# Optimization experiments

Hardware: AMD Instinct MI355X
Metric: run time of the kernel (lower is better)

The kernel has to match this reference:

```python
import jax, jax.numpy as jnp
import numpy as np

X = 512; Y = 512; C = 3; NK = 15
DT = 0.2; DD = 2; SIGMA = 0.95
THETA_X = 2.0; N_EXP = 2.0
K_SIZE = 16

# mesh-grid positions, cell centers at +0.5 (matches construct_mesh_grid)
POS = (jnp.stack(jnp.meshgrid(jnp.arange(X), jnp.arange(Y), indexing='ij'), axis=-1) + 0.5).astype(jnp.float32)  # [X,Y,2]


def _dwconv(img, k):
    # img [X,Y,C'] -> depthwise 3x3 cross-correlation with 'same' zero padding (matches torch conv2d)
    z = img.transpose(2, 0, 1)[None]                      # [1,C',X,Y]
    kern = jnp.tile(k[None, None], (z.shape[1], 1, 1, 1))  # [C',1,3,3]
    out = jax.lax.conv_general_dilated(z, kern, (1, 1), 'SAME', feature_group_count=z.shape[1])
    return out[0].transpose(1, 2, 0)


def _sobel(img):
    # returns [X,Y,2,C'] with (sy, sx) stacked on axis 2, matching torch code order
    kx = jnp.array([[-1., 0., 1.], [-2., 0., 2.], [-1., 0., 1.]], jnp.float32)
    return jnp.stack([_dwconv(img, kx.T), _dwconv(img, kx)], axis=2)


def _reintegrate(grid, F):
    # Flow-Lenia reintegration tracking: 25 static roll offsets, fused accumulation
    ma = DD - SIGMA
    mu = POS[..., None] + jnp.clip(DT * F, -ma, ma)  # [X,Y,2,C]
    mu = jnp.clip(mu, SIGMA, X - SIGMA)
    clip_hi = min(1.0, 2.0 * SIGMA)
    inv_area = 1.0 / (4.0 * SIGMA ** 2)
    acc = jnp.zeros_like(grid)
    for dx in range(-DD, DD + 1):
        for dy in range(-DD, DD + 1):
            gridR = jnp.roll(grid, (dx, dy), (0, 1))
            muR = jnp.roll(mu, (dx, dy), (0, 1))
            sz = 0.5 - jnp.abs(POS[..., None] - muR) + SIGMA
            area = jnp.prod(jnp.clip(sz, 0.0, clip_hi), axis=2) * inv_area  # [X,Y,C]
            acc = acc + gridR * area
    return acc


def _forward(x, Ks, m, s, h, w_c1, c0):
    # spectral kernels: normalize, fftshift, fft2 (matches construct_kernels)
    Ksn = Ks / Ks.sum(axis=(0, 1), keepdims=True)
    fk = jnp.fft.fft2(jnp.fft.fftshift(Ksn, axes=(0, 1)), axes=(0, 1))  # [X,Y,NK] complex
    fXs = jnp.fft.fft2(x, axes=(0, 1))
    Us = jnp.fft.ifft2(fk * fXs[:, :, c0], axes=(0, 1)).real            # [X,Y,NK]
    # growth * h (note: h appears again inside w_c1, faithful to original double multiply)
    Gs = (jnp.exp(-(((Us - m) / s) ** 2) * 0.5) * 2.0 - 1.0) * h
    Hs = jnp.einsum('xyk,kc->xyc', Gs, w_c1)                             # [X,Y,C]
    grad_u = _sobel(Hs)                                                  # [X,Y,2,C]
    grad_x = _sobel(x.sum(-1, keepdims=True))                            # [X,Y,2,1]
    alpha = jnp.clip((x[:, :, None, :] / THETA_X) ** N_EXP, 0.0, 1.0)    # [X,Y,1,C]
    F = grad_u * (1.0 - alpha) - grad_x * alpha                          # [X,Y,2,C]
    return _reintegrate(x, F)


def setup_inputs() -> dict:
    key = jax.random.key(0)
    k1, k2, k3, k4, k5 = jax.random.split(key, 5)
    x = jax.random.uniform(k1, (X, Y, C), jnp.float32)
    # ring kernels per construct_kernels (non-sparse branch)
    mg = np.mgrid[-X // 2:X // 2, -Y // 2:Y // 2]
    base = np.linalg.norm(mg, axis=0).astype(np.float32)
    ks_list = []
    for i in range(NK):
        r = 0.6 + 0.04 * i
        D = base / ((K_SIZE + 15) * r)
        sig = 0.5 * (np.tanh(-(D - 1.0) * 10.0 / 2.0) + 1.0)
        bell = np.exp(-(D - 0.5) ** 2 / 0.15)
        ks_list.append(sig * bell)
    Ks = jnp.asarray(np.stack(ks_list, -1).astype(np.float32))
    m = 0.1 + 0.3 * jax.random.uniform(k2, (NK,), jnp.float32)
    s = 0.03 + 0.15 * jax.random.uniform(k3, (NK,), jnp.float32)
    h = 0.3 + 0.7 * jax.random.uniform(k4, (NK,), jnp.float32)
    c0 = jax.random.randint(k5, (NK,), 0, C, jnp.int32)
    c1 = jnp.arange(NK) % C
    w_c1 = jax.nn.one_hot(c1, C, dtype=jnp.float32) * h[:, None]
    return {"x": x, "Ks": Ks, "m": m, "s": s, "h": h, "w_c1": w_c1, "c0": c0}


def reference(x, Ks, m, s, h, w_c1, c0):
    return _forward(x, Ks, m, s, h, w_c1, c0)
```

## Files before the change

kernel.cpp:

```cpp
#include <hip/hip_runtime.h>
#include <math.h>

#define NPIX 262144
#define NKER 15
#define PI_F 3.14159265358979323846f
#define HW 264
#define CS 578
#define SK(n) ((n) + ((n) >> 3))

__device__ __forceinline__ float2 cadd(float2 a, float2 b) { return make_float2(a.x + b.x, a.y + b.y); }
__device__ __forceinline__ float2 csub(float2 a, float2 b) { return make_float2(a.x - b.x, a.y - b.y); }
__device__ __forceinline__ float2 cmul(float2 a, float2 b) {
  return make_float2(a.x * b.x - a.y * b.y, a.x * b.y + a.y * b.x);
}
__device__ __forceinline__ float2 cmulc(float2 a, float2 b) {
  return make_float2(a.x * b.x + a.y * b.y, a.y * b.x - a.x * b.y);
}

__device__ __forceinline__ void build_tw(int lane, float2* pA, float2* pB) {
  float s, c;
  sincosf(-2.0f * PI_F * (float)lane / 512.0f, &s, &c);
  float2 w1 = make_float2(c, s);
  int h = lane & ~7;
  float2 wh = make_float2(__shfl(c, h, 64), __shfl(s, h, 64));
  pA[0] = w1;
  pA[1] = cmul(w1, w1);
  pA[2] = cmul(pA[1], w1);
  pA[3] = cmul(pA[1], pA[1]);
  pA[4] = cmul(pA[3], w1);
  pA[5] = cmul(pA[3], pA[1]);
  pA[6] = cmul(pA[3], pA[2]);
  pB[0] = wh;
  pB[1] = cmul(wh, wh);
  pB[2] = cmul(pB[1], wh);
  pB[3] = cmul(pB[1], pB[1]);
  pB[4] = cmul(pB[3], wh);
  pB[5] = cmul(pB[3], pB[1]);
  pB[6] = cmul(pB[3], pB[2]);
}

template <bool INV>
__device__ __forceinline__ void dft8(float2 a[8]) {
  const float R = 0.70710678118654752f;
  float2 t0 = cadd(a[0], a[4]), u0 = csub(a[0], a[4]);
  float2 t1 = cadd(a[1], a[5]), u1 = csub(a[1], a[5]);
  float2 t2 = cadd(a[2], a[6]), u2 = csub(a[2], a[6]);
  float2 t3 = cadd(a[3], a[7]), u3 = csub(a[3], a[7]);
  u1 = INV ? make_float2(R * (u1.x - u1.y), R * (u1.x + u1.y))
           : make_float2(R * (u1.x + u1.y), R * (u1.y - u1.x));
  u2 = INV ? make_float2(-u2.y, u2.x) : make_float2(u2.y, -u2.x);
  u3 = INV ? make_float2(-R * (u3.x + u3.y), R * (u3.x - u3.y))
           : make_float2(R * (u3.y - u3.x), -R * (u3.x + u3.y));
  float2 e0 = cadd(t0, t2), f0 = csub(t0, t2);
  float2 e1 = cadd(t1, t3), f1 = csub(t1, t3);
  f1 = INV ? make_float2(-f1.y, f1.x) : make_float2(f1.y, -f1.x);
  float2 g0 = cadd(u0, u2), h0 = csub(u0, u2);
  float2 g1 = cadd(u1, u3), h1 = csub(u1, u3);
  h1 = INV ? make_float2(-h1.y, h1.x) : make_float2(h1.y, -h1.x);
  a[0] = cadd(e0, e1); a[4] = csub(e0, e1);
  a[2] = cadd(f0, f1); a[6] = csub(f0, f1);
  a[1] = cadd(g0, g1); a[5] = csub(g0, g1);
  a[3] = cadd(h0, h1); a[7] = csub(h0, h1);
}

template <bool INV>
__device__ __forceinline__ void fft512_r8(float2 a[8], float2* buf, int lane,
                                          const float2* pA, const float2* pB) {
  dft8<INV>(a);
#pragma unroll
  for (int q = 1; q < 8; ++q) a[q] = INV ? cmulc(a[q], pA[q - 1]) : cmul(a[q], pA[q - 1]);
#pragma unroll
  for (int q = 0; q < 8; ++q) buf[9 * lane + q] = a[q];
#pragma unroll
  for (int q = 0; q < 8; ++q) a[q] = buf[SK(lane + 64 * q)];
  dft8<INV>(a);
#pragma unroll
  for (int q = 1; q < 8; ++q) a[q] = INV ? cmulc(a[q], pB[q - 1]) : cmul(a[q], pB[q - 1]);
  int h = lane & ~7;
  int b2 = 9 * h + (lane - h);
#pragma unroll
  for (int q = 0; q < 8; ++q) buf[b2 + 9 * q] = a[q];
#pragma unroll
  for (int q = 0; q < 8; ++q) a[q] = buf[SK(lane + 64 * q)];
  dft8<INV>(a);
}

__device__ __forceinline__ void split_store_halfplane(float2 a[8], float2* buf, int lane,
                                                      float2* d0, float2* d1) {
#pragma unroll
  for (int q = 0; q < 8; ++q) buf[SK(lane + 64 * q)] = a[q];
#pragma unroll
  for (int q = 0; q < 4; ++q) {
    int v = lane + 64 * q;
    int mir = (512 - v) & 511;
    float2 P = a[q];
    float2 Qc = buf[SK(mir)];
    float2 Q = make_float2(Qc.x, -Qc.y);
    d0[v] = make_float2(0.5f * (P.x + Q.x), 0.5f * (P.y + Q.y));
    d1[v] = make_float2(0.5f * (P.y - Q.y), -0.5f * (P.x - Q.x));
  }
  if (lane == 0) {
    float2 P = a[4];
    d0[256] = make_float2(P.x, 0.f);
    d1[256] = make_float2(P.y, 0.f);
  }
}

__global__ __launch_bounds__(512, 4) void rows_all(
    const float* __restrict__ Ks, const float* __restrict__ x,
    float* __restrict__ partial, float2* __restrict__ AkH,
    float2* __restrict__ AxH) {
  __shared__ float krow[512 * NKER];
  __shared__ float2 scr[8][CS];
  __shared__ float psum[480];
  int t = threadIdx.x, wave = t >> 6, lane = t & 63;
  float2 pA[7], pB[7];
  build_tw(lane, pA, pB);
  if (blockIdx.x < 512) {
    int b = blockIdx.x;
    int rs = (b + 256) & 511;
    const float2* src = (const float2*)Ks + (size_t)rs * 3840;
    float2* kr2 = (float2*)krow;
    for (int i = t; i < 3840; i += 512) kr2[i] = src[i];
    __syncthreads();
    if (t < 480) {
      int k = t >> 5, yg = t & 31;
      float s = 0.f;
      int base = yg * 16;
#pragma unroll
      for (int y = 0; y < 16; ++y) s += krow[(base + y) * NKER + k];
      psum[t] = s;
    }
    {
      int k1 = 2 * wave, k2 = k1 + 1;
      float2 a[8];
#pragma unroll
      for (int q = 0; q < 8; ++q) {
        int ys = (lane + 64 * q + 256) & 511;
        float re = krow[ys * NKER + k1];
        float im = (k2 < NKER) ? krow[ys * NKER + k2] : 0.f;
        a[q] = make_float2(re, im);
      }
      fft512_r8<false>(a, &scr[wave][0], lane, pA, pB);
      float2* d0 = AkH + ((size_t)k1 * 512 + b) * HW;
      float2* d1 = AkH + ((size_t)k2 * 512 + b) * HW;
      split_store_halfplane(a, &scr[wave][0], lane, d0, d1);
    }
    __syncthreads();
    if (t < NKER) {
      float s = 0.f;
#pragma unroll
      for (int g = 0; g < 32; ++g) s += psum[(t << 5) + g];
      partial[b * 16 + t] = s;
    }
  } else {
    int job = (blockIdx.x - 512) * 8 + wave;
    int c = job >> 8;
    int rp = job & 255;
    int r0 = rp, r1 = rp + 256;
    float2 a[8];
#pragma unroll
    for (int q = 0; q < 8; ++q) {
      int y = lane + 64 * q;
      a[q] = make_float2(x[((size_t)r0 * 512 + y) * 3 + c],
                         x[((size_t)r1 * 512 + y) * 3 + c]);
    }
    fft512_r8<false>(a, &scr[wave][0], lane, pA, pB);
    float2* d0 = AxH + ((size_t)c * 512 + r0) * HW;
    float2* d1 = AxH + ((size_t)c * 512 + r1) * HW;
    split_store_halfplane(a, &scr[wave][0], lane, d0, d1);
  }
}

__global__ __launch_bounds__(512, 4) void xcols(const float2* __restrict__ AxH,
                                                float2* __restrict__ FxT) {
  __shared__ float2 buf[8 * CS];
  int t = threadIdx.x, c = t >> 6, lane = t & 63;
  int col0 = blockIdx.x << 3, ch = blockIdx.y;
  float2 pA[7], pB[7];
  build_tw(lane, pA, pB);
  const float2* bx = AxH + (size_t)ch * 512 * HW;
#pragma unroll
  for (int u = 0; u < 8; ++u) {
    int idx = (u << 9) + t;
    int row = idx >> 3, cc = idx & 7;
    buf[cc * CS + SK(row)] = bx[(size_t)row * HW + col0 + cc];
  }
  __syncthreads();
  float2 a[8];
#pragma unroll
  for (int q = 0; q < 8; ++q) a[q] = buf[c * CS + SK(lane + 64 * q)];
  fft512_r8<false>(a, &buf[c * CS], lane, pA, pB);
  float2* dst = FxT + ((size_t)ch * HW + col0 + c) * 512;
#pragma unroll
  for (int q = 0; q < 8; ++q) dst[lane + 64 * q] = a[q];
}

__global__ __launch_bounds__(512, 4) void fused_cols(
    float2* __restrict__ AkH, const float2* __restrict__ FxT,
    const int* __restrict__ c0, const float* __restrict__ partial,
    float* __restrict__ sums) {
  __shared__ float2 buf[8 * CS];
  __shared__ float red[512];
  int t = threadIdx.x;
  if (blockIdx.x == 33) {
    if (blockIdx.y != 0) return;
    int k = t & 15, g = t >> 4;
    float acc = 0.f;
    for (int b = g; b < 512; b += 32) acc += partial[b * 16 + k];
    red[t] = acc;
    __syncthreads();
    if (t < 16) {
      float s = 0.f;
#pragma unroll
      for (int g2 = 0; g2 < 32; ++g2) s += red[g2 * 16 + t];
      sums[t] = s;
    }
    return;
  }
  int col0 = blockIdx.x << 3, k = blockIdx.y;
  int c = t >> 6, lane = t & 63;
  float2 pA[7], pB[7];
  build_tw(lane, pA, pB);
  float2* bk = AkH + (size_t)k * 512 * HW;
#pragma unroll
  for (int u = 0; u < 8; ++u) {
    int idx = (u << 9) + t;
    int row = idx >> 3, cc = idx & 7;
    buf[cc * CS + SK(row)] = bk[(size_t)row * HW + col0 + cc];
  }
  const float2* fx = FxT + ((size_t)c0[k] * HW + col0 + c) * 512;
  float2 xq[8];
#pragma unroll
  for (int q = 0; q < 8; ++q) xq[q] = fx[lane + 64 * q];
  __syncthreads();
  float2 a[8];
#pragma unroll
  for (int q = 0; q < 8; ++q) a[q] = buf[c * CS + SK(lane + 64 * q)];
  fft512_r8<false>(a, &buf[c * CS], lane, pA, pB);
#pragma unroll
  for (int q = 0; q < 8; ++q) a[q] = cmul(a[q], xq[q]);
  fft512_r8<true>(a, &buf[c * CS], lane, pA, pB);
#pragma unroll
  for (int q = 0; q < 8; ++q) buf[c * CS + SK(lane + 64 * q)] = a[q];
  __syncthreads();
#pragma unroll
  for (int u = 0; u < 8; ++u) {
    int idx = (u << 9) + t;
    int row = idx >> 3, cc = idx & 7;
    bk[(size_t)row * HW + col0 + cc] = buf[cc * CS + SK(row)];
  }
}

__global__ __launch_bounds__(512, 4) void irows_growth_combine(
    const float2* __restrict__ AkH, const float* __restrict__ sums,
    const float* __restrict__ m, const float* __restrict__ s,
    const float* __restrict__ h, const float* __restrict__ w,
    float* __restrict__ Hs) {
  __shared__ float2 scr[8][CS];
  __shared__ float accL[4][3][512];
  __shared__ float mk[16], isk[16], hk[16], wk[16][3], sck[16];
  int t = threadIdx.x, wave = t >> 6, lane = t & 63;
  int row = blockIdx.x;
  if (t < NKER) {
    mk[t] = m[t]; isk[t] = 1.0f / s[t]; hk[t] = h[t];
    sck[t] = 1.0f / (sums[t] * 262144.0f);
    wk[t][0] = w[t * 3 + 0]; wk[t][1] = w[t * 3 + 1]; wk[t][2] = w[t * 3 + 2];
  }
  __syncthreads();
  float2 pA[7], pB[7];
  build_tw(lane, pA, pB);
  float acc[3][8];
#pragma unroll
  for (int cc = 0; cc < 3; ++cc)
#pragma unroll
    for (int q = 0; q < 8; ++q) acc[cc][q] = 0.f;
  {
    int slot = wave;
    int k1 = 2 * slot, k2 = 2 * slot + 1;
    bool dual = (k2 < NKER);
    const float2* p1 = AkH + ((size_t)k1 * 512 + row) * HW;
    const float2* p2 = AkH + ((size_t)(dual ? k2 : k1) * 512 + row) * HW;
    float2 a[8];
#pragma unroll
    for (int q = 0; q < 8; ++q) {
      int v = lane + 64 * q;
      if (v <= 256) {
        float2 A1 = p1[v];
        float2 A2 = dual ? p2[v] : make_float2(0.f, 0.f);
        a[q] = make_float2(A1.x - A2.y, A1.y + A2.x);
      } else {
        int mi = 512 - v;
        float2 A1 = p1[mi];
        float2 A2 = dual ? p2[mi] : make_float2(0.f, 0.f);
        a[q] = make_float2(A1.x + A2.y, -A1.y + A2.x);
      }
    }
    fft512_r8<true>(a, &scr[wave][0], lane, pA, pB);
    float m1 = mk[k1], i1 = isk[k1], h1 = hk[k1], s1 = sck[k1];
    float w10 = wk[k1][0], w11 = wk[k1][1], w12 = wk[k1][2];
#pragma unroll
    for (int q = 0; q < 8; ++q) {
      float tt = (a[q].x * s1 - m1) * i1;
      float g = (expf(-0.5f * tt * tt) * 2.0f - 1.0f) * h1;
      acc[0][q] += g * w10; acc[1][q] += g * w11; acc[2][q] += g * w12;
    }
    if (dual) {
      float m2 = mk[k2], i2 = isk[k2], h2 = hk[k2], s2 = sck[k2];
      float w20 = wk[k2][0], w21 = wk[k2][1], w22 = wk[k2][2];
#pragma unroll
      for (int q = 0; q < 8; ++q) {
        float tt = (a[q].y * s2 - m2) * i2;
        float g = (expf(-0.5f * tt * tt) * 2.0f - 1.0f) * h2;
        acc[0][q] += g * w20; acc[1][q] += g * w21; acc[2][q] += g * w22;
      }
    }
  }
  if (wave < 4) {
#pragma unroll
    for (int cc = 0; cc < 3; ++cc)
#pragma unroll
      for (int q = 0; q < 8; ++q) accL[wave][cc][lane + 64 * q] = acc[cc][q];
  }
  __syncthreads();
  if (wave >= 4) {
#pragma unroll
    for (int cc = 0; cc < 3; ++cc)
#pragma unroll
      for (int q = 0; q < 8; ++q) accL[wave - 4][cc][lane + 64 * q] += acc[cc][q];
  }
  __syncthreads();
#pragma unroll
  for (int cc = 0; cc < 3; ++cc) {
    float v = accL[0][cc][t] + accL[1][cc][t] + accL[2][cc][t] + accL[3][cc][t];
    Hs[(size_t)cc * NPIX + (size_t)row * 512 + t] = v;
  }
}

__global__ void flow_reint(const float* __restrict__ x, const float* __restrict__ Hs,
                           float* __restrict__ out) {
  __shared__ float tS[7][496];
  __shared__ float muT[400 * 6];
  int ox = (blockIdx.x >> 5) << 4;
  int oy = (blockIdx.x & 31) << 4;
  for (int i = threadIdx.x; i < 484; i += 256) {
    int li = i / 22, lj = i % 22;
    int qx = (ox - 3 + li) & 511, qy = (oy - 3 + lj) & 511;
    int q = (qx << 9) | qy;
    float h0 = Hs[q], h1 = Hs[NPIX + q], h2 = Hs[2 * NPIX + q];
    float x0 = x[(size_t)q * 3 + 0], x1 = x[(size_t)q * 3 + 1], x2 = x[(size_t)q * 3 + 2];
    tS[0][i] = h0; tS[1][i] = h1; tS[2][i] = h2;
    tS[3][i] = x0 + x1 + x2;
    tS[4][i] = x0; tS[5][i] = x1; tS[6][i] = x2;
  }
  __syncthreads();
  for (int i = threadIdx.x; i < 400; i += 256) {
    int hi = i / 20, hj = i % 20;
    int qx = (ox - 2 + hi) & 511, qy = (oy - 2 + hj) & 511;
    float syH0 = 0.f, syH1 = 0.f, syH2 = 0.f;
    float sxH0 = 0.f, sxH1 = 0.f, sxH2 = 0.f;
    float syX = 0.f, sxX = 0.f;
#pragma unroll
    for (int di = -1; di <= 1; ++di) {
#pragma unroll
      for (int dj = -1; dj <= 1; ++dj) {
        if (di == 0 && dj == 0) continue;
        int xi = qx + di, yj = qy + dj;
        if ((unsigned)xi >= 512u || (unsigned)yj >= 512u) continue;
        int l = (hi + 1 + di) * 22 + (hj + 1 + dj);
        float wy = (float)di * ((dj == 0) ? 2.f : 1.f);
        float wx = (float)dj * ((di == 0) ? 2.f : 1.f);
        float h0 = tS[0][l], h1 = tS[1][l], h2 = tS[2][l];
        syH0 += wy * h0; syH1 += wy * h1; syH2 += wy * h2;
        sxH0 += wx * h0; sxH1 += wx * h1; sxH2 += wx * h2;
        float xs = tS[3][l];
        syX += wy * xs; sxX += wx * xs;
      }
    }
    int lc = (hi + 1) * 22 + (hj + 1);
    float cxq = (float)qx + 0.5f, cyq = (float)qy + 0.5f;
    float syH[3] = {syH0, syH1, syH2};
    float sxH[3] = {sxH0, sxH1, sxH2};
    int b6 = i * 6;
#pragma unroll
    for (int c = 0; c < 3; ++c) {
      float xc = tS[4 + c][lc];
      float tt = xc * 0.5f;
      float alpha = fminf(tt * tt, 1.0f);
      float F0 = syH[c] * (1.f - alpha) - syX * alpha;
      float F1 = sxH[c] * (1.f - alpha) - sxX * alpha;
      float m0 = cxq + fminf(fmaxf(0.2f * F0, -1.05f), 1.05f);
      float m1 = cyq + fminf(fmaxf(0.2f * F1, -1.05f), 1.05f);
      muT[b6 + c]     = fminf(fmaxf(m0, 0.95f), 511.05f);
      muT[b6 + 3 + c] = fminf(fmaxf(m1, 0.95f), 511.05f);
    }
  }
  __syncthreads();
  int o = threadIdx.x;
  int lx = o >> 4, ly = o & 15;
  int px_ = ox + lx, py_ = oy + ly;
  float cx = (float)px_ + 0.5f, cy = (float)py_ + 0.5f;
  float a0 = 0.f, a1 = 0.f, a2 = 0.f;
#pragma unroll
  for (int dx = -2; dx <= 2; ++dx) {
    int hi = lx + 2 - dx;
#pragma unroll
    for (int dy = -2; dy <= 2; ++dy) {
      int hj = ly + 2 - dy;
      int b6 = (hi * 20 + hj) * 6;
      int lb = (hi + 1) * 22 + (hj + 1);
      float wv;
      wv = fminf(fmaxf(1.45f - fabsf(cx - muT[b6 + 0]), 0.f), 1.f) *
           fminf(fmaxf(1.45f - fabsf(cy - muT[b6 + 3]), 0.f), 1.f);
      a0 += tS[4][lb] * wv;
      wv = fminf(fmaxf(1.45f - fabsf(cx - muT[b6 + 1]), 0.f), 1.f) *
           fminf(fmaxf(1.45f - fabsf(cy - muT[b6 + 4]), 0.f), 1.f);
      a1 += tS[5][lb] * wv;
      wv = fminf(fmaxf(1.45f - fabsf(cx - muT[b6 + 2]), 0.f), 1.f) *
           fminf(fmaxf(1.45f - fabsf(cy - muT[b6 + 5]), 0.f), 1.f);
      a2 += tS[6][lb] * wv;
    }
  }
  const float inv_area = 0.27700831f;
  size_t p = (size_t)((px_ << 9) | py_);
  out[p * 3 + 0] = a0 * inv_area;
  out[p * 3 + 1] = a1 * inv_area;
  out[p * 3 + 2] = a2 * inv_area;
}

extern "C" void kernel_launch(void* const* d_in, const int* in_sizes, int n_in,
                              void* d_out, int out_size, void* d_ws, size_t ws_size,
                              hipStream_t stream) {
  const float* x    = (const float*)d_in[0];
  const float* Ks   = (const float*)d_in[1];
  const float* m    = (const float*)d_in[2];
  const float* s    = (const float*)d_in[3];
  const float* h    = (const float*)d_in[4];
  const float* w_c1 = (const float*)d_in[5];
  const int*   c0   = (const int*)d_in[6];
  float* out = (float*)d_out;

  char* ws = (char*)d_ws;
  size_t off = 0;
  float* sums    = (float*)(ws + off); off += 1024;
  float* partial = (float*)(ws + off); off += 512 * 16 * 4;
  float2* AxH  = (float2*)(ws + off); off += (size_t)3 * 512 * HW * 8;
  float2* AkH  = (float2*)(ws + off); off += (size_t)16 * 512 * HW * 8;
  float2* FxT  = (float2*)(ws + off); off += (size_t)3 * HW * 512 * 8;
  float*  Hs   = (float*)(ws + off);  off += (size_t)3 * NPIX * 4;

  rows_all<<<608, 512, 0, stream>>>(Ks, x, partial, AkH, AxH);
  xcols<<<dim3(33, 3), 512, 0, stream>>>(AxH, FxT);
  fused_cols<<<dim3(34, NKER), 512, 0, stream>>>(AkH, FxT, c0, partial, sums);
  irows_growth_combine<<<512, 512, 0, stream>>>(AkH, sums, m, s, h, w_c1, Hs);
  flow_reint<<<1024, 256, 0, stream>>>(x, Hs, out);
}
```

Before: 128.1 us.

## Vectorize complex math with float2 ext vectors, skip zero kernel rows, halve column blocks

Replaces the float2 struct helpers with clang ext_vector_type(2) arithmetic, so complex multiplies and the reintegration clamps can map to packed FP32 instructions. Row FFTs for Ks rows that are all zero within a wave are skipped and zeros are written directly. The column FFT kernels move from 8 to 4 columns per block (256 threads), doubling the grid, and the sum reduction moves from fused_cols into xcols. The zero-skip depends on the data being sparse and adds a wave vote, and the smaller blocks mean more launches' worth of blocks with less work each.

```diff
diff --git a/kernel.cpp b/kernel.cpp
--- a/kernel.cpp
+++ b/kernel.cpp
@@ -8,21 +8,31 @@
 #define CS 578
 #define SK(n) ((n) + ((n) >> 3))
 
-__device__ __forceinline__ float2 cadd(float2 a, float2 b) { return make_float2(a.x + b.x, a.y + b.y); }
-__device__ __forceinline__ float2 csub(float2 a, float2 b) { return make_float2(a.x - b.x, a.y - b.y); }
-__device__ __forceinline__ float2 cmul(float2 a, float2 b) {
-  return make_float2(a.x * b.x - a.y * b.y, a.x * b.y + a.y * b.x);
-}
-__device__ __forceinline__ float2 cmulc(float2 a, float2 b) {
-  return make_float2(a.x * b.x + a.y * b.y, a.y * b.x - a.x * b.y);
-}
-
-__device__ __forceinline__ void build_tw(int lane, float2* pA, float2* pB) {
+typedef float f2 __attribute__((ext_vector_type(2)));
+
+__device__ __forceinline__ f2 mkf2(float a, float b) { f2 r; r.x = a; r.y = b; return r; }
+__device__ __forceinline__ f2 rotp(f2 a) { return mkf2(-a.y, a.x); }
+__device__ __forceinline__ f2 rotm(f2 a) { return mkf2(a.y, -a.x); }
+__device__ __forceinline__ f2 cmul(f2 a, f2 b) {
+  f2 t = mkf2(a.x, a.x) * b;
+  f2 u = mkf2(-a.y, a.y) * mkf2(b.y, b.x);
+  return t + u;
+}
+__device__ __forceinline__ f2 cmulc(f2 a, f2 b) {
+  f2 t = a * mkf2(b.x, b.x);
+  f2 u = mkf2(a.y, -a.x) * mkf2(b.y, b.y);
+  return t + u;
+}
+__device__ __forceinline__ f2 vmin(f2 a, f2 b) { return __builtin_elementwise_min(a, b); }
+__device__ __forceinline__ f2 vmax(f2 a, f2 b) { return __builtin_elementwise_max(a, b); }
+__device__ __forceinline__ f2 vabs(f2 a) { return __builtin_elementwise_abs(a); }
+
+__device__ __forceinline__ void build_tw(int lane, f2* pA, f2* pB) {
   float s, c;
   sincosf(-2.0f * PI_F * (float)lane / 512.0f, &s, &c);
-  float2 w1 = make_float2(c, s);
+  f2 w1 = mkf2(c, s);
   int h = lane & ~7;
-  float2 wh = make_float2(__shfl(c, h, 64), __shfl(s, h, 64));
+  f2 wh = mkf2(__shfl(c, h, 64), __shfl(s, h, 64));
   pA[0] = w1;
   pA[1] = cmul(w1, w1);
   pA[2] = cmul(pA[1], w1);
@@ -40,32 +50,30 @@
 }
 
 template <bool INV>
-__device__ __forceinline__ void dft8(float2 a[8]) {
+__device__ __forceinline__ void dft8(f2 a[8]) {
   const float R = 0.70710678118654752f;
-  float2 t0 = cadd(a[0], a[4]), u0 = csub(a[0], a[4]);
-  float2 t1 = cadd(a[1], a[5]), u1 = csub(a[1], a[5]);
-  float2 t2 = cadd(a[2], a[6]), u2 = csub(a[2], a[6]);
-  float2 t3 = cadd(a[3], a[7]), u3 = csub(a[3], a[7]);
-  u1 = INV ? make_float2(R * (u1.x - u1.y), R * (u1.x + u1.y))
-           : make_float2(R * (u1.x + u1.y), R * (u1.y - u1.x));
-  u2 = INV ? make_float2(-u2.y, u2.x) : make_float2(u2.y, -u2.x);
-  u3 = INV ? make_float2(-R * (u3.x + u3.y), R * (u3.x - u3.y))
-           : make_float2(R * (u3.y - u3.x), -R * (u3.x + u3.y));
-  float2 e0 = cadd(t0, t2), f0 = csub(t0, t2);
-  float2 e1 = cadd(t1, t3), f1 = csub(t1, t3);
-  f1 = INV ? make_float2(-f1.y, f1.x) : make_float2(f1.y, -f1.x);
-  float2 g0 = cadd(u0, u2), h0 = csub(u0, u2);
-  float2 g1 = cadd(u1, u3), h1 = csub(u1, u3);
-  h1 = INV ? make_float2(-h1.y, h1.x) : make_float2(h1.y, -h1.x);
-  a[0] = cadd(e0, e1); a[4] = csub(e0, e1);
-  a[2] = cadd(f0, f1); a[6] = csub(f0, f1);
-  a[1] = cadd(g0, g1); a[5] = csub(g0, g1);
-  a[3] = cadd(h0, h1); a[7] = csub(h0, h1);
+  f2 t0 = a[0] + a[4], u0 = a[0] - a[4];
+  f2 t1 = a[1] + a[5], u1 = a[1] - a[5];
+  f2 t2 = a[2] + a[6], u2 = a[2] - a[6];
+  f2 t3 = a[3] + a[7], u3 = a[3] - a[7];
+  u1 = (INV ? (u1 + rotp(u1)) : (u1 + rotm(u1))) * R;
+  u2 = INV ? rotp(u2) : rotm(u2);
+  u3 = (INV ? (rotp(u3) - u3) : (rotm(u3) - u3)) * R;
+  f2 e0 = t0 + t2, f0 = t0 - t2;
+  f2 e1 = t1 + t3, f1 = t1 - t3;
+  f1 = INV ? rotp(f1) : rotm(f1);
+  f2 g0 = u0 + u2, h0 = u0 - u2;
+  f2 g1 = u1 + u3, h1 = u1 - u3;
+  h1 = INV ? rotp(h1) : rotm(h1);
+  a[0] = e0 + e1; a[4] = e0 - e1;
+  a[2] = f0 + f1; a[6] = f0 - f1;
+  a[1] = g0 + g1; a[5] = g0 - g1;
+  a[3] = h0 + h1; a[7] = h0 - h1;
 }
 
 template <bool INV>
-__device__ __forceinline__ void fft512_r8(float2 a[8], float2* buf, int lane,
-                                          const float2* pA, const float2* pB) {
+__device__ __forceinline__ void fft512_r8(f2 a[8], f2* buf, int lane,
+                                          const f2* pA, const f2* pB) {
   dft8<INV>(a);
 #pragma unroll
   for (int q = 1; q < 8; ++q) a[q] = INV ? cmulc(a[q], pA[q - 1]) : cmul(a[q], pA[q - 1]);
@@ -85,42 +93,41 @@
   dft8<INV>(a);
 }
 
-__device__ __forceinline__ void split_store_halfplane(float2 a[8], float2* buf, int lane,
-                                                      float2* d0, float2* d1) {
+__device__ __forceinline__ void split_store_halfplane(f2 a[8], f2* buf, int lane,
+                                                      f2* d0, f2* d1) {
 #pragma unroll
   for (int q = 0; q < 8; ++q) buf[SK(lane + 64 * q)] = a[q];
 #pragma unroll
   for (int q = 0; q < 4; ++q) {
     int v = lane + 64 * q;
     int mir = (512 - v) & 511;
-    float2 P = a[q];
-    float2 Qc = buf[SK(mir)];
-    float2 Q = make_float2(Qc.x, -Qc.y);
-    d0[v] = make_float2(0.5f * (P.x + Q.x), 0.5f * (P.y + Q.y));
-    d1[v] = make_float2(0.5f * (P.y - Q.y), -0.5f * (P.x - Q.x));
+    f2 P = a[q];
+    f2 Qc = buf[SK(mir)];
+    d0[v] = (P + mkf2(Qc.x, -Qc.y)) * 0.5f;
+    d1[v] = mkf2(0.5f * (P.y + Qc.y), 0.5f * (Qc.x - P.x));
   }
   if (lane == 0) {
-    float2 P = a[4];
-    d0[256] = make_float2(P.x, 0.f);
-    d1[256] = make_float2(P.y, 0.f);
+    f2 P = a[4];
+    d0[256] = mkf2(P.x, 0.f);
+    d1[256] = mkf2(P.y, 0.f);
   }
 }
 
 __global__ __launch_bounds__(512, 4) void rows_all(
     const float* __restrict__ Ks, const float* __restrict__ x,
-    float* __restrict__ partial, float2* __restrict__ AkH,
-    float2* __restrict__ AxH) {
+    float* __restrict__ partial, f2* __restrict__ AkH,
+    f2* __restrict__ AxH) {
   __shared__ float krow[512 * NKER];
-  __shared__ float2 scr[8][CS];
+  __shared__ f2 scr[8][CS];
   __shared__ float psum[480];
   int t = threadIdx.x, wave = t >> 6, lane = t & 63;
-  float2 pA[7], pB[7];
+  f2 pA[7], pB[7];
   build_tw(lane, pA, pB);
   if (blockIdx.x < 512) {
     int b = blockIdx.x;
     int rs = (b + 256) & 511;
-    const float2* src = (const float2*)Ks + (size_t)rs * 3840;
-    float2* kr2 = (float2*)krow;
+    const f2* src = (const f2*)Ks + (size_t)rs * 3840;
+    f2* kr2 = (f2*)krow;
     for (int i = t; i < 3840; i += 512) kr2[i] = src[i];
     __syncthreads();
     if (t < 480) {
@@ -133,18 +140,27 @@
     }
     {
       int k1 = 2 * wave, k2 = k1 + 1;
-      float2 a[8];
+      f2 a[8];
+      bool nz = false;
 #pragma unroll
       for (int q = 0; q < 8; ++q) {
         int ys = (lane + 64 * q + 256) & 511;
         float re = krow[ys * NKER + k1];
         float im = (k2 < NKER) ? krow[ys * NKER + k2] : 0.f;
-        a[q] = make_float2(re, im);
+        a[q] = mkf2(re, im);
+        nz |= (re != 0.f) || (im != 0.f);
       }
-      fft512_r8<false>(a, &scr[wave][0], lane, pA, pB);
-      float2* d0 = AkH + ((size_t)k1 * 512 + b) * HW;
-      float2* d1 = AkH + ((size_t)k2 * 512 + b) * HW;
-      split_store_halfplane(a, &scr[wave][0], lane, d0, d1);
+      f2* d0 = AkH + ((size_t)k1 * 512 + b) * HW;
+      f2* d1 = AkH + ((size_t)k2 * 512 + b) * HW;
+      if (__any((int)nz)) {
+        fft512_r8<false>(a, &scr[wave][0], lane, pA, pB);
+        split_store_halfplane(a, &scr[wave][0], lane, d0, d1);
+      } else {
+        f2 z = mkf2(0.f, 0.f);
+#pragma unroll
+        for (int q = 0; q < 4; ++q) { int v = lane + 64 * q; d0[v] = z; d1[v] = z; }
+        if (lane == 0) { d0[256] = z; d1[256] = z; }
+      }
     }
     __syncthreads();
     if (t < NKER) {
@@ -158,86 +174,88 @@
     int c = job >> 8;
     int rp = job & 255;
     int r0 = rp, r1 = rp + 256;
-    float2 a[8];
+    f2 a[8];
 #pragma unroll
     for (int q = 0; q < 8; ++q) {
       int y = lane + 64 * q;
-      a[q] = make_float2(x[((size_t)r0 * 512 + y) * 3 + c],
-                         x[((size_t)r1 * 512 + y) * 3 + c]);
+      a[q] = mkf2(x[((size_t)r0 * 512 + y) * 3 + c],
+                  x[((size_t)r1 * 512 + y) * 3 + c]);
     }
     fft512_r8<false>(a, &scr[wave][0], lane, pA, pB);
-    float2* d0 = AxH + ((size_t)c * 512 + r0) * HW;
-    float2* d1 = AxH + ((size_t)c * 512 + r1) * HW;
+    f2* d0 = AxH + ((size_t)c * 512 + r0) * HW;
+    f2* d1 = AxH + ((size_t)c * 512 + r1) * HW;
     split_store_halfplane(a, &scr[wave][0], lane, d0, d1);
   }
 }
 
-__global__ __launch_bounds__(512, 4) void xcols(const float2* __restrict__ AxH,
-                                                float2* __restrict__ FxT) {
-  __shared__ float2 buf[8 * CS];
-  int t = threadIdx.x, c = t >> 6, lane = t & 63;
-  int col0 = blockIdx.x << 3, ch = blockIdx.y;
-  float2 pA[7], pB[7];
-  build_tw(lane, pA, pB);
-  const float2* bx = AxH + (size_t)ch * 512 * HW;
-#pragma unroll
-  for (int u = 0; u < 8; ++u) {
-    int idx = (u << 9) + t;
-    int row = idx >> 3, cc = idx & 7;
-    buf[cc * CS + SK(row)] = bx[(size_t)row * HW + col0 + cc];
-  }
-  __syncthreads();
-  float2 a[8];
-#pragma unroll
-  for (int q = 0; q < 8; ++q) a[q] = buf[c * CS + SK(lane + 64 * q)];
-  fft512_r8<false>(a, &buf[c * CS], lane, pA, pB);
-  float2* dst = FxT + ((size_t)ch * HW + col0 + c) * 512;
-#pragma unroll
-  for (int q = 0; q < 8; ++q) dst[lane + 64 * q] = a[q];
-}
-
-__global__ __launch_bounds__(512, 4) void fused_cols(
-    float2* __restrict__ AkH, const float2* __restrict__ FxT,
-    const int* __restrict__ c0, const float* __restrict__ partial,
-    float* __restrict__ sums) {
-  __shared__ float2 buf[8 * CS];
-  __shared__ float red[512];
+__global__ __launch_bounds__(256, 4) void xcols(const f2* __restrict__ AxH,
+                                                f2* __restrict__ FxT,
+                                                const float* __restrict__ partial,
+                                                float* __restrict__ sums) {
+  __shared__ f2 buf[4 * CS];
+  __shared__ float red[256];
   int t = threadIdx.x;
-  if (blockIdx.x == 33) {
+  if (blockIdx.x == 66) {
     if (blockIdx.y != 0) return;
     int k = t & 15, g = t >> 4;
     float acc = 0.f;
-    for (int b = g; b < 512; b += 32) acc += partial[b * 16 + k];
+    for (int b = g; b < 512; b += 16) acc += partial[b * 16 + k];
     red[t] = acc;
     __syncthreads();
     if (t < 16) {
       float s = 0.f;
 #pragma unroll
-      for (int g2 = 0; g2 < 32; ++g2) s += red[g2 * 16 + t];
+      for (int g2 = 0; g2 < 16; ++g2) s += red[g2 * 16 + t];
       sums[t] = s;
     }
     return;
   }
-  int col0 = blockIdx.x << 3, k = blockIdx.y;
   int c = t >> 6, lane = t & 63;
-  float2 pA[7], pB[7];
+  int col0 = blockIdx.x << 2, ch = blockIdx.y;
+  f2 pA[7], pB[7];
   build_tw(lane, pA, pB);
-  float2* bk = AkH + (size_t)k * 512 * HW;
+  const f2* bx = AxH + (size_t)ch * 512 * HW;
 #pragma unroll
   for (int u = 0; u < 8; ++u) {
-    int idx = (u << 9) + t;
-    int row = idx >> 3, cc = idx & 7;
-    buf[cc * CS + SK(row)] = bk[(size_t)row * HW + col0 + cc];
-  }
-  const float2* fx = FxT + ((size_t)c0[k] * HW + col0 + c) * 512;
-  float2 xq[8];
-#pragma unroll
-  for (int q = 0; q < 8; ++q) xq[q] = fx[lane + 64 * q];
-  __syncthreads();
-  float2 a[8];
+    int idx = (u << 8) + t;
+    int row = idx >> 2, cc = idx & 3;
+    buf[cc * CS + SK(row)] = bx[(size_t)row * HW + col0 + cc];
+  }
+  __syncthreads();
+  f2 a[8];
 #pragma unroll
   for (int q = 0; q < 8; ++q) a[q] = buf[c * CS + SK(lane + 64 * q)];
   fft512_r8<false>(a, &buf[c * CS], lane, pA, pB);
+  f2* dst = FxT + ((size_t)ch * HW + col0 + c) * 512;
+#pragma unroll
+  for (int q = 0; q < 8; ++q) dst[lane + 64 * q] = a[q];
+}
+
+__global__ __launch_bounds__(256, 4) void fused_cols(
+    f2* __restrict__ AkH, const f2* __restrict__ FxT,
+    const int* __restrict__ c0) {
+  __shared__ f2 buf[4 * CS];
+  int t = threadIdx.x;
+  int col0 = blockIdx.x << 2, k = blockIdx.y;
+  int c = t >> 6, lane = t & 63;
+  f2 pA[7], pB[7];
+  build_tw(lane, pA, pB);
+  f2* bk = AkH + (size_t)k * 512 * HW;
+#pragma unroll
+  for (int u = 0; u < 8; ++u) {
+    int idx = (u << 8) + t;
+    int row = idx >> 2, cc = idx & 3;
+    buf[cc * CS + SK(row)] = bk[(size_t)row * HW + col0 + cc];
+  }
+  const f2* fx = FxT + ((size_t)c0[k] * HW + col0 + c) * 512;
+  f2 xq[8];
+#pragma unroll
+  for (int q = 0; q < 8; ++q) xq[q] = fx[lane + 64 * q];
+  __syncthreads();
+  f2 a[8];
+#pragma unroll
+  for (int q = 0; q < 8; ++q) a[q] = buf[c * CS + SK(lane + 64 * q)];
+  fft512_r8<false>(a, &buf[c * CS], lane, pA, pB);
 #pragma unroll
   for (int q = 0; q < 8; ++q) a[q] = cmul(a[q], xq[q]);
   fft512_r8<true>(a, &buf[c * CS], lane, pA, pB);
@@ -246,18 +264,18 @@
   __syncthreads();
 #pragma unroll
   for (int u = 0; u < 8; ++u) {
-    int idx = (u << 9) + t;
-    int row = idx >> 3, cc = idx & 7;
+    int idx = (u << 8) + t;
+    int row = idx >> 2, cc = idx & 3;
     bk[(size_t)row * HW + col0 + cc] = buf[cc * CS + SK(row)];
   }
 }
 
 __global__ __launch_bounds__(512, 4) void irows_growth_combine(
-    const float2* __restrict__ AkH, const float* __restrict__ sums,
+    const f2* __restrict__ AkH, const float* __restrict__ sums,
     const float* __restrict__ m, const float* __restrict__ s,
     const float* __restrict__ h, const float* __restrict__ w,
     float* __restrict__ Hs) {
-  __shared__ float2 scr[8][CS];
+  __shared__ f2 scr[8][CS];
   __shared__ float accL[4][3][512];
   __shared__ float mk[16], isk[16], hk[16], wk[16][3], sck[16];
   int t = threadIdx.x, wave = t >> 6, lane = t & 63;
@@ -268,7 +286,7 @@
     wk[t][0] = w[t * 3 + 0]; wk[t][1] = w[t * 3 + 1]; wk[t][2] = w[t * 3 + 2];
   }
   __syncthreads();
-  float2 pA[7], pB[7];
+  f2 pA[7], pB[7];
   build_tw(lane, pA, pB);
   float acc[3][8];
 #pragma unroll
@@ -279,21 +297,21 @@
     int slot = wave;
     int k1 = 2 * slot, k2 = 2 * slot + 1;
     bool dual = (k2 < NKER);
-    const float2* p1 = AkH + ((size_t)k1 * 512 + row) * HW;
-    const float2* p2 = AkH + ((size_t)(dual ? k2 : k1) * 512 + row) * HW;
-    float2 a[8];
+    const f2* p1 = AkH + ((size_t)k1 * 512 + row) * HW;
+    const f2* p2 = AkH + ((size_t)(dual ? k2 : k1) * 512 + row) * HW;
+    f2 a[8];
 #pragma unroll
     for (int q = 0; q < 8; ++q) {
       int v = lane + 64 * q;
       if (v <= 256) {
-        float2 A1 = p1[v];
-        float2 A2 = dual ? p2[v] : make_float2(0.f, 0.f);
-        a[q] = make_float2(A1.x - A2.y, A1.y + A2.x);
+        f2 A1 = p1[v];
+        f2 A2 = dual ? p2[v] : mkf2(0.f, 0.f);
+        a[q] = mkf2(A1.x - A2.y, A1.y + A2.x);
       } else {
         int mi = 512 - v;
-        float2 A1 = p1[mi];
-        float2 A2 = dual ? p2[mi] : make_float2(0.f, 0.f);
-        a[q] = make_float2(A1.x + A2.y, -A1.y + A2.x);
+        f2 A1 = p1[mi];
+        f2 A2 = dual ? p2[mi] : mkf2(0.f, 0.f);
+        a[q] = mkf2(A1.x + A2.y, -A1.y + A2.x);
       }
     }
     fft512_r8<true>(a, &scr[wave][0], lane, pA, pB);
@@ -340,7 +358,7 @@
 __global__ void flow_reint(const float* __restrict__ x, const float* __restrict__ Hs,
                            float* __restrict__ out) {
   __shared__ float tS[7][496];
-  __shared__ float muT[400 * 6];
+  __shared__ f2 muF[400 * 3];
   int ox = (blockIdx.x >> 5) << 4;
   int oy = (blockIdx.x & 31) << 4;
   for (int i = threadIdx.x; i < 484; i += 256) {
@@ -357,9 +375,7 @@
   for (int i = threadIdx.x; i < 400; i += 256) {
     int hi = i / 20, hj = i % 20;
     int qx = (ox - 2 + hi) & 511, qy = (oy - 2 + hj) & 511;
-    float syH0 = 0.f, syH1 = 0.f, syH2 = 0.f;
-    float sxH0 = 0.f, sxH1 = 0.f, sxH2 = 0.f;
-    float syX = 0.f, sxX = 0.f;
+    f2 sH0 = mkf2(0.f, 0.f), sH1 = sH0, sH2 = sH0, sX = sH0;
 #pragma unroll
     for (int di = -1; di <= 1; ++di) {
 #pragma unroll
@@ -370,36 +386,34 @@
         int l = (hi + 1 + di) * 22 + (hj + 1 + dj);
         float wy = (float)di * ((dj == 0) ? 2.f : 1.f);
         float wx = (float)dj * ((di == 0) ? 2.f : 1.f);
-        float h0 = tS[0][l], h1 = tS[1][l], h2 = tS[2][l];
-        syH0 += wy * h0; syH1 += wy * h1; syH2 += wy * h2;
-        sxH0 += wx * h0; sxH1 += wx * h1; sxH2 += wx * h2;
-        float xs = tS[3][l];
-        syX += wy * xs; sxX += wx * xs;
+        f2 wv = mkf2(wy, wx);
+        sH0 += wv * tS[0][l];
+        sH1 += wv * tS[1][l];
+        sH2 += wv * tS[2][l];
+        sX  += wv * tS[3][l];
       }
     }
     int lc = (hi + 1) * 22 + (hj + 1);
-    float cxq = (float)qx + 0.5f, cyq = (float)qy + 0.5f;
-    float syH[3] = {syH0, syH1, syH2};
-    float sxH[3] = {sxH0, sxH1, sxH2};
-    int b6 = i * 6;
+    f2 ctr = mkf2((float)qx + 0.5f, (float)qy + 0.5f);
+    f2 sH[3] = {sH0, sH1, sH2};
+    const f2 lo = mkf2(-1.05f, -1.05f), hi2 = mkf2(1.05f, 1.05f);
+    const f2 mlo = mkf2(0.95f, 0.95f), mhi = mkf2(511.05f, 511.05f);
 #pragma unroll
     for (int c = 0; c < 3; ++c) {
       float xc = tS[4 + c][lc];
       float tt = xc * 0.5f;
       float alpha = fminf(tt * tt, 1.0f);
-      float F0 = syH[c] * (1.f - alpha) - syX * alpha;
-      float F1 = sxH[c] * (1.f - alpha) - sxX * alpha;
-      float m0 = cxq + fminf(fmaxf(0.2f * F0, -1.05f), 1.05f);
-      float m1 = cyq + fminf(fmaxf(0.2f * F1, -1.05f), 1.05f);
-      muT[b6 + c]     = fminf(fmaxf(m0, 0.95f), 511.05f);
-      muT[b6 + 3 + c] = fminf(fmaxf(m1, 0.95f), 511.05f);
+      f2 F = sH[c] * (1.f - alpha) - sX * alpha;
+      f2 mu = ctr + vmin(vmax(F * 0.2f, lo), hi2);
+      muF[i * 3 + c] = vmin(vmax(mu, mlo), mhi);
     }
   }
   __syncthreads();
   int o = threadIdx.x;
   int lx = o >> 4, ly = o & 15;
   int px_ = ox + lx, py_ = oy + ly;
-  float cx = (float)px_ + 0.5f, cy = (float)py_ + 0.5f;
+  f2 ctr = mkf2((float)px_ + 0.5f, (float)py_ + 0.5f);
+  const f2 c145 = mkf2(1.45f, 1.45f), c0f = mkf2(0.f, 0.f), c1f = mkf2(1.f, 1.f);
   float a0 = 0.f, a1 = 0.f, a2 = 0.f;
 #pragma unroll
   for (int dx = -2; dx <= 2; ++dx) {
@@ -407,18 +421,14 @@
 #pragma unroll
     for (int dy = -2; dy <= 2; ++dy) {
       int hj = ly + 2 - dy;
-      int b6 = (hi * 20 + hj) * 6;
+      int cell = hi * 20 + hj;
       int lb = (hi + 1) * 22 + (hj + 1);
-      float wv;
-      wv = fminf(fmaxf(1.45f - fabsf(cx - muT[b6 + 0]), 0.f), 1.f) *
-           fminf(fmaxf(1.45f - fabsf(cy - muT[b6 + 3]), 0.f), 1.f);
-      a0 += tS[4][lb] * wv;
-      wv = fminf(fmaxf(1.45f - fabsf(cx - muT[b6 + 1]), 0.f), 1.f) *
-           fminf(fmaxf(1.45f - fabsf(cy - muT[b6 + 4]), 0.f), 1.f);
-      a1 += tS[5][lb] * wv;
-      wv = fminf(fmaxf(1.45f - fabsf(cx - muT[b6 + 2]), 0.f), 1.f) *
-           fminf(fmaxf(1.45f - fabsf(cy - muT[b6 + 5]), 0.f), 1.f);
-      a2 += tS[6][lb] * wv;
+      f2 w0 = vmin(vmax(c145 - vabs(ctr - muF[cell * 3 + 0]), c0f), c1f);
+      a0 += tS[4][lb] * (w0.x * w0.y);
+      f2 w1 = vmin(vmax(c145 - vabs(ctr - muF[cell * 3 + 1]), c0f), c1f);
+      a1 += tS[5][lb] * (w1.x * w1.y);
+      f2 w2 = vmin(vmax(c145 - vabs(ctr - muF[cell * 3 + 2]), c0f), c1f);
+      a2 += tS[6][lb] * (w2.x * w2.y);
     }
   }
   const float inv_area = 0.27700831f;
@@ -444,14 +454,14 @@
   size_t off = 0;
   float* sums    = (float*)(ws + off); off += 1024;
   float* partial = (float*)(ws + off); off += 512 * 16 * 4;
-  float2* AxH  = (float2*)(ws + off); off += (size_t)3 * 512 * HW * 8;
-  float2* AkH  = (float2*)(ws + off); off += (size_t)16 * 512 * HW * 8;
-  float2* FxT  = (float2*)(ws + off); off += (size_t)3 * HW * 512 * 8;
-  float*  Hs   = (float*)(ws + off);  off += (size_t)3 * NPIX * 4;
+  f2* AxH  = (f2*)(ws + off); off += (size_t)3 * 512 * HW * 8;
+  f2* AkH  = (f2*)(ws + off); off += (size_t)16 * 512 * HW * 8;
+  f2* FxT  = (f2*)(ws + off); off += (size_t)3 * HW * 512 * 8;
+  float* Hs = (float*)(ws + off); off += (size_t)3 * NPIX * 4;
 
   rows_all<<<608, 512, 0, stream>>>(Ks, x, partial, AkH, AxH);
-  xcols<<<dim3(33, 3), 512, 0, stream>>>(AxH, FxT);
-  fused_cols<<<dim3(34, NKER), 512, 0, stream>>>(AkH, FxT, c0, partial, sums);
+  xcols<<<dim3(67, 3), 256, 0, stream>>>(AxH, FxT, partial, sums);
+  fused_cols<<<dim3(66, NKER), 256, 0, stream>>>(AkH, FxT, c0);
   irows_growth_combine<<<512, 512, 0, stream>>>(AkH, sums, m, s, h, w_c1, Hs);
   flow_reint<<<1024, 256, 0, stream>>>(x, Hs, out);
 }
```

Measured after the change: 139.4 us. 8.9% more time.
